# Kernel tuning notes

Hardware: AMD Instinct MI355X
Metric: run time of the kernel (lower is better)

The kernel has to match this reference:

```python
import jax, jax.numpy as jnp
import numpy as np

BN_EPS = 1e-5


def setup_inputs() -> dict:
    key = jax.random.key(0)
    k1, k2, k3 = jax.random.split(key, 3)
    B, T, V, Cin, Cout = 32, 256, 86, 64, 128
    x = jax.random.normal(k1, (B, T, V, Cin), dtype=jnp.float32)
    # random sparse symmetric 0/1 adjacency (no self loops; forward adds I)
    a = (jax.random.uniform(k2, (V, V)) < 0.08).astype(jnp.float32)
    adj = jnp.clip(a + a.T, 0.0, 1.0) * (1.0 - jnp.eye(V, dtype=jnp.float32))
    # kaiming_uniform_(a=sqrt(5)) on [Cin, Cout]: bound = sqrt(6/((1+5)*Cin)) = 1/sqrt(Cin)
    bound = 1.0 / np.sqrt(Cin)
    w = jax.random.uniform(k3, (Cin, Cout), minval=-bound, maxval=bound, dtype=jnp.float32)
    gamma = jnp.ones((Cout,), dtype=jnp.float32)
    beta = jnp.zeros((Cout,), dtype=jnp.float32)
    return {"x": x, "adj": adj, "w": w, "gamma": gamma, "beta": beta}


def reference(x, adj, w, gamma, beta):
    # x: [B, T, V, Cin]
    V = adj.shape[0]
    a = adj + jnp.eye(V, dtype=adj.dtype)
    deg_inv_sqrt = a.sum(axis=1) ** -0.5                      # [V]
    norm_adj = deg_inv_sqrt[:, None] * a * deg_inv_sqrt[None, :]
    # graph aggregation + feature transform (permute-free, fused einsums)
    y = jnp.einsum('uv,btvc->btuc', norm_adj, x)              # [B,T,V,Cin]
    y = jnp.einsum('btvc,cd->btvd', y, w)                     # [B,T,V,Cout]
    # BatchNorm2d (training mode): per-channel stats over (B,T,V)
    mean = y.mean(axis=(0, 1, 2))
    var = y.var(axis=(0, 1, 2))                               # biased, as in BN
    y = (y - mean) * jax.lax.rsqrt(var + BN_EPS) * gamma + beta
    return jax.nn.relu(y)                                     # [B,T,V,Cout]
```

## Files before the change

kernel.cpp:

```cpp
#include <hip/hip_runtime.h>

#define V 86
#define VP 96
#define CIN 64
#define COUT 128
#define BT 8192
#define NSTAT (32*256*86)

#define OFF_FLAG  0
#define OFF_NADJ  512
#define OFF_WT    19456
#define OFF_GSUM  35840
#define OFF_GSQ   36352
#define OFF_SCALE 36864
#define OFF_SHIFT 37376

typedef short short8 __attribute__((ext_vector_type(8)));
typedef float float4v __attribute__((ext_vector_type(4)));

static __device__ __forceinline__ float bf2f(ushort u) {
    union { uint i; float f; } c; c.i = ((uint)u) << 16; return c.f;
}
static __device__ __forceinline__ ushort f2bf(float f) {
    union { float f; uint i; } c; c.f = f;
    uint u = c.i;
    uint r = u + 0x7FFFu + ((u >> 16) & 1u);
    return (ushort)(r >> 16);
}
static __device__ __forceinline__ uint packbf(float a, float b) {
    return (uint)f2bf(a) | ((uint)f2bf(b) << 16);
}
template<bool BF>
static __device__ __forceinline__ float ldg(const void* p, int i) {
    if (BF) return bf2f(((const ushort*)p)[i]);
    else    return ((const float*)p)[i];
}

__global__ void k0_detect(const uint* __restrict__ adj_raw, char* __restrict__ ws) {
    __shared__ int s_found;
    if (threadIdx.x == 0) s_found = 0;
    __syncthreads();
    int found = 0;
    for (int i = threadIdx.x; i < 3698; i += blockDim.x) {
        uint wd = adj_raw[i];
        if (wd == 0x00003F80u || wd == 0x3F803F80u) found = 1;
    }
    if (found) atomicOr(&s_found, 1);
    __syncthreads();
    if (threadIdx.x == 0) *(int*)(ws + OFF_FLAG) = s_found;
}

template<bool BF>
__global__ void k1_prep(const void* __restrict__ adj, const void* __restrict__ w,
                        char* __restrict__ ws) {
    const int flag = *(const volatile int*)(ws + OFF_FLAG);
    if ((flag != 0) != BF) return;
    __shared__ float dinv[V];
    const int t = threadIdx.x;
    ushort* nadj = (ushort*)(ws + OFF_NADJ);
    ushort* wT   = (ushort*)(ws + OFF_WT);
    float*  gsum = (float*)(ws + OFF_GSUM);
    float*  gsq  = (float*)(ws + OFF_GSQ);

    if (t < V) {
        float s = 0.f;
        for (int v2 = 0; v2 < V; ++v2)
            s += ldg<BF>(adj, t * V + v2) + (v2 == t ? 1.f : 0.f);
        dinv[t] = rsqrtf(s);
    }
    __syncthreads();
    for (int i = t; i < VP * VP; i += blockDim.x) {
        int u = i / VP, v2 = i % VP;
        float val = 0.f;
        if (u < V && v2 < V) {
            float a = ldg<BF>(adj, u * V + v2) + (v2 == u ? 1.f : 0.f);
            val = dinv[u] * a * dinv[v2];
        }
        nadj[i] = f2bf(val);
    }
    for (int i = t; i < CIN * COUT; i += blockDim.x) {
        int cc = i >> 7, d = i & 127;
        wT[d * CIN + cc] = BF ? ((const ushort*)w)[i] : f2bf(((const float*)w)[i]);
    }
    if (t < COUT) { gsum[t] = 0.f; gsq[t] = 0.f; }
}

#define NJ_STR 104
#define XS_STR 72
#define YT_STR 104

template<bool BF, bool STATS>
__global__ __launch_bounds__(512, 4) void k2_pass(const void* __restrict__ x,
                                                  char* __restrict__ ws,
                                                  void* __restrict__ outv) {
    const int flag = *(const volatile int*)(ws + OFF_FLAG);
    if ((flag != 0) != BF) return;

    __shared__ __align__(16) short s_nadj[VP * NJ_STR];
    __shared__ __align__(16) short s_x[VP * XS_STR];
    __shared__ __align__(16) short s_yT[COUT * YT_STR];

    const int tid  = threadIdx.x;
    const int lane = tid & 63, wv = tid >> 6;
    const int col  = lane & 15, quad = lane >> 4;
    const int d_own = wv * 16 + col;

    {
        const ushort* g = (const ushort*)(ws + OFF_NADJ);
        for (int i = tid; i < VP * 12; i += 512) {
            int r = i / 12, j = i % 12;
            *(uint4*)&s_nadj[r * NJ_STR + j * 8] = *(const uint4*)&g[r * VP + j * 8];
        }
    }
    short8 bw[2];
    {
        const ushort* wt = (const ushort*)(ws + OFF_WT);
        bw[0] = *(const short8*)&wt[d_own * CIN + quad * 8];
        bw[1] = *(const short8*)&wt[d_own * CIN + 32 + quad * 8];
    }
    if (tid < 160) {
        int r = V + (tid >> 4), j = tid & 15;
        *(uint2*)&s_x[r * XS_STR + j * 4] = (uint2){0u, 0u};
    }
    float sc = 0.f, sh = 0.f;
    if (!STATS) {
        sc = ((const float*)(ws + OFF_SCALE))[d_own];
        sh = ((const float*)(ws + OFF_SHIFT))[d_own];
    }
    float s1 = 0.f, s2 = 0.f;

    for (int ib = 0; ib < 8; ++ib) {
        const int bt = blockIdx.x * 8 + ib;
        __syncthreads();

        if (BF) {
            const ushort* xg = (const ushort*)x + (size_t)bt * (V * CIN);
            for (int i = tid; i < V * 8; i += 512) {
                int r = i >> 3, j = i & 7;
                *(uint4*)&s_x[r * XS_STR + j * 8] = *(const uint4*)&xg[r * CIN + j * 8];
            }
        } else {
            const float* xg = (const float*)x + (size_t)bt * (V * CIN);
            for (int i = tid; i < V * 16; i += 512) {
                int r = i >> 4, j = i & 15;
                float4 f = *(const float4*)&xg[r * CIN + j * 4];
                uint2 o; o.x = packbf(f.x, f.y); o.y = packbf(f.z, f.w);
                *(uint2*)&s_x[r * XS_STR + j * 4] = o;
            }
        }
        __syncthreads();

        float4v accy[6];
        #pragma unroll
        for (int m = 0; m < 6; ++m) accy[m] = (float4v){0.f, 0.f, 0.f, 0.f};
        #pragma unroll
        for (int ks = 0; ks < 2; ++ks) {
            #pragma unroll
            for (int m = 0; m < 6; ++m) {
                short8 ax = *(const short8*)&s_x[(m * 16 + col) * XS_STR + ks * 32 + quad * 8];
                accy[m] = __builtin_amdgcn_mfma_f32_16x16x32_bf16(ax, bw[ks], accy[m], 0, 0, 0);
            }
        }
        #pragma unroll
        for (int m = 0; m < 6; ++m)
            #pragma unroll
            for (int r = 0; r < 4; ++r)
                s_yT[d_own * YT_STR + m * 16 + quad * 4 + r] = (short)f2bf(accy[m][r]);
        __syncthreads();

        float4v accz[6];
        #pragma unroll
        for (int m = 0; m < 6; ++m) accz[m] = (float4v){0.f, 0.f, 0.f, 0.f};
        #pragma unroll
        for (int ks = 0; ks < 3; ++ks) {
            short8 by = *(const short8*)&s_yT[d_own * YT_STR + ks * 32 + quad * 8];
            #pragma unroll
            for (int m = 0; m < 6; ++m) {
                short8 an = *(const short8*)&s_nadj[(m * 16 + col) * NJ_STR + ks * 32 + quad * 8];
                accz[m] = __builtin_amdgcn_mfma_f32_16x16x32_bf16(an, by, accz[m], 0, 0, 0);
            }
        }

        if (STATS) {
            #pragma unroll
            for (int m = 0; m < 6; ++m)
                #pragma unroll
                for (int r = 0; r < 4; ++r) {
                    int u = m * 16 + quad * 4 + r;
                    if (u < V) { float v2 = accz[m][r]; s1 += v2; s2 += v2 * v2; }
                }
        } else {
            const size_t base = (size_t)bt * (V * COUT) + d_own;
            #pragma unroll
            for (int m = 0; m < 6; ++m)
                #pragma unroll
                for (int r = 0; r < 4; ++r) {
                    int u = m * 16 + quad * 4 + r;
                    if (u < V) {
                        float val = fmaxf(accz[m][r] * sc + sh, 0.f);
                        if (BF) ((ushort*)outv)[base + (size_t)u * COUT] = f2bf(val);
                        else    ((float*)outv)[base + (size_t)u * COUT]  = val;
                    }
                }
        }
    }

    if (STATS) {
        s1 += __shfl_xor(s1, 16); s1 += __shfl_xor(s1, 32);
        s2 += __shfl_xor(s2, 16); s2 += __shfl_xor(s2, 32);
        if (quad == 0) {
            atomicAdd((float*)(ws + OFF_GSUM) + d_own, s1);
            atomicAdd((float*)(ws + OFF_GSQ)  + d_own, s2);
        }
    }
}

template<bool BF>
__global__ void k3_finalize(const void* __restrict__ gamma, const void* __restrict__ beta,
                            char* __restrict__ ws) {
    const int flag = *(const volatile int*)(ws + OFF_FLAG);
    if ((flag != 0) != BF) return;
    int d = threadIdx.x;
    if (d < COUT) {
        const float* gsum = (const float*)(ws + OFF_GSUM);
        const float* gsq  = (const float*)(ws + OFF_GSQ);
        float* scale = (float*)(ws + OFF_SCALE);
        float* shift = (float*)(ws + OFF_SHIFT);
        const float inv_n = 1.f / (float)NSTAT;
        float mean = gsum[d] * inv_n;
        float var  = gsq[d] * inv_n - mean * mean;
        float s    = ldg<BF>(gamma, d) * rsqrtf(var + 1e-5f);
        scale[d] = s;
        shift[d] = ldg<BF>(beta, d) - mean * s;
    }
}

extern "C" void kernel_launch(void* const* d_in, const int* in_sizes, int n_in,
                              void* d_out, int out_size, void* d_ws, size_t ws_size,
                              hipStream_t stream) {
    const void* x     = d_in[0];
    const void* adj   = d_in[1];
    const void* w     = d_in[2];
    const void* gamma = d_in[3];
    const void* beta  = d_in[4];
    char* ws = (char*)d_ws;

    hipLaunchKernelGGL(k0_detect, dim3(1), dim3(256), 0, stream, (const uint*)adj, ws);
    hipLaunchKernelGGL((k1_prep<true>),  dim3(1), dim3(256), 0, stream, adj, w, ws);
    hipLaunchKernelGGL((k1_prep<false>), dim3(1), dim3(256), 0, stream, adj, w, ws);
    hipLaunchKernelGGL((k2_pass<true,  true>),  dim3(1024), dim3(512), 0, stream, x, ws, d_out);
    hipLaunchKernelGGL((k2_pass<false, true>),  dim3(1024), dim3(512), 0, stream, x, ws, d_out);
    hipLaunchKernelGGL((k3_finalize<true>),  dim3(1), dim3(128), 0, stream, gamma, beta, ws);
    hipLaunchKernelGGL((k3_finalize<false>), dim3(1), dim3(128), 0, stream, gamma, beta, ws);
    hipLaunchKernelGGL((k2_pass<true,  false>), dim3(1024), dim3(512), 0, stream, x, ws, d_out);
    hipLaunchKernelGGL((k2_pass<false, false>), dim3(1024), dim3(512), 0, stream, x, ws, d_out);
}
```

Baseline: 613.7 us.

## Store pre-BN output in stats pass and apply BN in elementwise kernel

The stats pass now writes the raw aggregated-and-transformed values to the output buffer while accumulating channel statistics. A new vectorized elementwise kernel then applies scale, shift and ReLU in place. This replaces the second full recomputation pass, removing its re-read of x and its duplicate MFMA work. In exchange, the output is written and then read back and rewritten, which adds memory traffic.

```diff
diff --git a/kernel.cpp b/kernel.cpp
--- a/kernel.cpp
+++ b/kernel.cpp
@@ -4,7 +4,6 @@
 #define VP 96
 #define CIN 64
 #define COUT 128
-#define BT 8192
 #define NSTAT (32*256*86)
 
 #define OFF_FLAG  0
@@ -182,12 +181,18 @@
         }
 
         if (STATS) {
+            const size_t base = (size_t)bt * (V * COUT) + d_own;
             #pragma unroll
             for (int m = 0; m < 6; ++m)
                 #pragma unroll
                 for (int r = 0; r < 4; ++r) {
                     int u = m * 16 + quad * 4 + r;
-                    if (u < V) { float v2 = accz[m][r]; s1 += v2; s2 += v2 * v2; }
+                    if (u < V) {
+                        float v2 = accz[m][r];
+                        s1 += v2; s2 += v2 * v2;
+                        if (BF) ((ushort*)outv)[base + (size_t)u * COUT] = f2bf(v2);
+                        else    ((float*)outv)[base + (size_t)u * COUT]  = v2;
+                    }
                 }
         } else {
             const size_t base = (size_t)bt * (V * COUT) + d_own;
@@ -235,6 +240,55 @@
     }
 }
 
+template<bool BF>
+__global__ __launch_bounds__(256) void k4_bn(char* __restrict__ ws, void* __restrict__ outv) {
+    const int flag = *(const volatile int*)(ws + OFF_FLAG);
+    if ((flag != 0) != BF) return;
+    const float* scale = (const float*)(ws + OFF_SCALE);
+    const float* shift = (const float*)(ws + OFF_SHIFT);
+    const int d8 = threadIdx.x & 15;
+    float sc[8], sh[8];
+    #pragma unroll
+    for (int j = 0; j < 8; ++j) { sc[j] = scale[d8 * 8 + j]; sh[j] = shift[d8 * 8 + j]; }
+    const int nrows = 8192 * V;
+    const int rstride = (gridDim.x * blockDim.x) >> 4;
+    int row = (blockIdx.x * blockDim.x + threadIdx.x) >> 4;
+    for (; row < nrows; row += rstride) {
+        if (BF) {
+            uint4* p = (uint4*)((ushort*)outv + (size_t)row * COUT + d8 * 8);
+            uint4 v = *p;
+            float f0 = bf2f((ushort)v.x), f1 = bf2f((ushort)(v.x >> 16));
+            float f2 = bf2f((ushort)v.y), f3 = bf2f((ushort)(v.y >> 16));
+            float f4 = bf2f((ushort)v.z), f5 = bf2f((ushort)(v.z >> 16));
+            float f6 = bf2f((ushort)v.w), f7 = bf2f((ushort)(v.w >> 16));
+            f0 = fmaxf(fmaf(f0, sc[0], sh[0]), 0.f);
+            f1 = fmaxf(fmaf(f1, sc[1], sh[1]), 0.f);
+            f2 = fmaxf(fmaf(f2, sc[2], sh[2]), 0.f);
+            f3 = fmaxf(fmaf(f3, sc[3], sh[3]), 0.f);
+            f4 = fmaxf(fmaf(f4, sc[4], sh[4]), 0.f);
+            f5 = fmaxf(fmaf(f5, sc[5], sh[5]), 0.f);
+            f6 = fmaxf(fmaf(f6, sc[6], sh[6]), 0.f);
+            f7 = fmaxf(fmaf(f7, sc[7], sh[7]), 0.f);
+            uint4 o;
+            o.x = packbf(f0, f1); o.y = packbf(f2, f3);
+            o.z = packbf(f4, f5); o.w = packbf(f6, f7);
+            *p = o;
+        } else {
+            float4* p = (float4*)((float*)outv + (size_t)row * COUT + d8 * 8);
+            float4 a = p[0], b = p[1];
+            a.x = fmaxf(fmaf(a.x, sc[0], sh[0]), 0.f);
+            a.y = fmaxf(fmaf(a.y, sc[1], sh[1]), 0.f);
+            a.z = fmaxf(fmaf(a.z, sc[2], sh[2]), 0.f);
+            a.w = fmaxf(fmaf(a.w, sc[3], sh[3]), 0.f);
+            b.x = fmaxf(fmaf(b.x, sc[4], sh[4]), 0.f);
+            b.y = fmaxf(fmaf(b.y, sc[5], sh[5]), 0.f);
+            b.z = fmaxf(fmaf(b.z, sc[6], sh[6]), 0.f);
+            b.w = fmaxf(fmaf(b.w, sc[7], sh[7]), 0.f);
+            p[0] = a; p[1] = b;
+        }
+    }
+}
+
 extern "C" void kernel_launch(void* const* d_in, const int* in_sizes, int n_in,
                               void* d_out, int out_size, void* d_ws, size_t ws_size,
                               hipStream_t stream) {
@@ -252,6 +306,6 @@
     hipLaunchKernelGGL((k2_pass<false, true>),  dim3(1024), dim3(512), 0, stream, x, ws, d_out);
     hipLaunchKernelGGL((k3_finalize<true>),  dim3(1), dim3(128), 0, stream, gamma, beta, ws);
     hipLaunchKernelGGL((k3_finalize<false>), dim3(1), dim3(128), 0, stream, gamma, beta, ws);
-    hipLaunchKernelGGL((k2_pass<true,  false>), dim3(1024), dim3(512), 0, stream, x, ws, d_out);
-    hipLaunchKernelGGL((k2_pass<false, false>), dim3(1024), dim3(512), 0, stream, x, ws, d_out);
-}
+    hipLaunchKernelGGL((k4_bn<true>),  dim3(2048), dim3(256), 0, stream, ws, d_out);
+    hipLaunchKernelGGL((k4_bn<false>), dim3(2048), dim3(256), 0, stream, ws, d_out);
+}
```

New measurement: 691.6 us. 1.13x slower.

## Stage two time slices per barrier, drop intra-wave sync, skip unused dtype launches

Applied to the files above, without the earlier changes.

The main kernel now loads two (b,t) slices of x into a doubled shared buffer per iteration. This halves the outer loop count and its block-wide barriers. The barrier between writing and reading the transposed intermediate is removed, which relies on each wave touching only its own rows. The padding-row check in the stats accumulation is dropped because padded rows are zero. On the host, input byte sizes decide whether the bf16 or f32 kernel variants need launching, so launches that would return immediately are skipped. This saves launch overhead but raises shared memory use per block.

```diff
diff --git a/kernel.cpp b/kernel.cpp
--- a/kernel.cpp
+++ b/kernel.cpp
@@ -97,7 +97,7 @@
     if ((flag != 0) != BF) return;
 
     __shared__ __align__(16) short s_nadj[VP * NJ_STR];
-    __shared__ __align__(16) short s_x[VP * XS_STR];
+    __shared__ __align__(16) short s_x[2 * VP * XS_STR];
     __shared__ __align__(16) short s_yT[COUT * YT_STR];
 
     const int tid  = threadIdx.x;
@@ -121,6 +121,7 @@
     if (tid < 160) {
         int r = V + (tid >> 4), j = tid & 15;
         *(uint2*)&s_x[r * XS_STR + j * 4] = (uint2){0u, 0u};
+        *(uint2*)&s_x[VP * XS_STR + r * XS_STR + j * 4] = (uint2){0u, 0u};
     }
     float sc = 0.f, sh = 0.f;
     if (!STATS) {
@@ -129,79 +130,88 @@
     }
     float s1 = 0.f, s2 = 0.f;
 
-    for (int ib = 0; ib < 8; ++ib) {
-        const int bt = blockIdx.x * 8 + ib;
+    for (int ip = 0; ip < 4; ++ip) {
+        const int btp = blockIdx.x * 8 + ip * 2;
         __syncthreads();
 
-        if (BF) {
-            const ushort* xg = (const ushort*)x + (size_t)bt * (V * CIN);
-            for (int i = tid; i < V * 8; i += 512) {
-                int r = i >> 3, j = i & 7;
-                *(uint4*)&s_x[r * XS_STR + j * 8] = *(const uint4*)&xg[r * CIN + j * 8];
-            }
-        } else {
-            const float* xg = (const float*)x + (size_t)bt * (V * CIN);
-            for (int i = tid; i < V * 16; i += 512) {
-                int r = i >> 4, j = i & 15;
-                float4 f = *(const float4*)&xg[r * CIN + j * 4];
-                uint2 o; o.x = packbf(f.x, f.y); o.y = packbf(f.z, f.w);
-                *(uint2*)&s_x[r * XS_STR + j * 4] = o;
+        #pragma unroll
+        for (int h = 0; h < 2; ++h) {
+            short* sx = s_x + h * (VP * XS_STR);
+            if (BF) {
+                const ushort* xg = (const ushort*)x + (size_t)(btp + h) * (V * CIN);
+                for (int i = tid; i < V * 8; i += 512) {
+                    int r = i >> 3, j = i & 7;
+                    *(uint4*)&sx[r * XS_STR + j * 8] = *(const uint4*)&xg[r * CIN + j * 8];
+                }
+            } else {
+                const float* xg = (const float*)x + (size_t)(btp + h) * (V * CIN);
+                for (int i = tid; i < V * 16; i += 512) {
+                    int r = i >> 4, j = i & 15;
+                    float4 f = *(const float4*)&xg[r * CIN + j * 4];
+                    uint2 o; o.x = packbf(f.x, f.y); o.y = packbf(f.z, f.w);
+                    *(uint2*)&sx[r * XS_STR + j * 4] = o;
+                }
             }
         }
         __syncthreads();
 
-        float4v accy[6];
         #pragma unroll
-        for (int m = 0; m < 6; ++m) accy[m] = (float4v){0.f, 0.f, 0.f, 0.f};
-        #pragma unroll
-        for (int ks = 0; ks < 2; ++ks) {
-            #pragma unroll
-            for (int m = 0; m < 6; ++m) {
-                short8 ax = *(const short8*)&s_x[(m * 16 + col) * XS_STR + ks * 32 + quad * 8];
-                accy[m] = __builtin_amdgcn_mfma_f32_16x16x32_bf16(ax, bw[ks], accy[m], 0, 0, 0);
-            }
-        }
-        #pragma unroll
-        for (int m = 0; m < 6; ++m)
-            #pragma unroll
-            for (int r = 0; r < 4; ++r)
-                s_yT[d_own * YT_STR + m * 16 + quad * 4 + r] = (short)f2bf(accy[m][r]);
-        __syncthreads();
-
-        float4v accz[6];
-        #pragma unroll
-        for (int m = 0; m < 6; ++m) accz[m] = (float4v){0.f, 0.f, 0.f, 0.f};
-        #pragma unroll
-        for (int ks = 0; ks < 3; ++ks) {
-            short8 by = *(const short8*)&s_yT[d_own * YT_STR + ks * 32 + quad * 8];
-            #pragma unroll
-            for (int m = 0; m < 6; ++m) {
-                short8 an = *(const short8*)&s_nadj[(m * 16 + col) * NJ_STR + ks * 32 + quad * 8];
-                accz[m] = __builtin_amdgcn_mfma_f32_16x16x32_bf16(an, by, accz[m], 0, 0, 0);
-            }
-        }
-
-        if (STATS) {
+        for (int h = 0; h < 2; ++h) {
+            const short* sx = s_x + h * (VP * XS_STR);
+            const int bt = btp + h;
+
+            float4v accy[6];
+            #pragma unroll
+            for (int m = 0; m < 6; ++m) accy[m] = (float4v){0.f, 0.f, 0.f, 0.f};
+            #pragma unroll
+            for (int ks = 0; ks < 2; ++ks) {
+                #pragma unroll
+                for (int m = 0; m < 6; ++m) {
+                    short8 ax = *(const short8*)&sx[(m * 16 + col) * XS_STR + ks * 32 + quad * 8];
+                    accy[m] = __builtin_amdgcn_mfma_f32_16x16x32_bf16(ax, bw[ks], accy[m], 0, 0, 0);
+                }
+            }
             #pragma unroll
             for (int m = 0; m < 6; ++m)
                 #pragma unroll
-                for (int r = 0; r < 4; ++r) {
-                    int u = m * 16 + quad * 4 + r;
-                    if (u < V) { float v2 = accz[m][r]; s1 += v2; s2 += v2 * v2; }
-                }
-        } else {
-            const size_t base = (size_t)bt * (V * COUT) + d_own;
-            #pragma unroll
-            for (int m = 0; m < 6; ++m)
-                #pragma unroll
-                for (int r = 0; r < 4; ++r) {
-                    int u = m * 16 + quad * 4 + r;
-                    if (u < V) {
-                        float val = fmaxf(accz[m][r] * sc + sh, 0.f);
-                        if (BF) ((ushort*)outv)[base + (size_t)u * COUT] = f2bf(val);
-                        else    ((float*)outv)[base + (size_t)u * COUT]  = val;
+                for (int r = 0; r < 4; ++r)
+                    s_yT[d_own * YT_STR + m * 16 + quad * 4 + r] = (short)f2bf(accy[m][r]);
+
+            float4v accz[6];
+            #pragma unroll
+            for (int m = 0; m < 6; ++m) accz[m] = (float4v){0.f, 0.f, 0.f, 0.f};
+            #pragma unroll
+            for (int ks = 0; ks < 3; ++ks) {
+                short8 by = *(const short8*)&s_yT[d_own * YT_STR + ks * 32 + quad * 8];
+                #pragma unroll
+                for (int m = 0; m < 6; ++m) {
+                    short8 an = *(const short8*)&s_nadj[(m * 16 + col) * NJ_STR + ks * 32 + quad * 8];
+                    accz[m] = __builtin_amdgcn_mfma_f32_16x16x32_bf16(an, by, accz[m], 0, 0, 0);
+                }
+            }
+
+            if (STATS) {
+                #pragma unroll
+                for (int m = 0; m < 6; ++m)
+                    #pragma unroll
+                    for (int r = 0; r < 4; ++r) {
+                        float v2 = accz[m][r];
+                        s1 += v2; s2 += v2 * v2;
                     }
-                }
+            } else {
+                const size_t base = (size_t)bt * (V * COUT) + d_own;
+                #pragma unroll
+                for (int m = 0; m < 6; ++m)
+                    #pragma unroll
+                    for (int r = 0; r < 4; ++r) {
+                        int u = m * 16 + quad * 4 + r;
+                        if (u < V) {
+                            float val = fmaxf(accz[m][r] * sc + sh, 0.f);
+                            if (BF) ((ushort*)outv)[base + (size_t)u * COUT] = f2bf(val);
+                            else    ((float*)outv)[base + (size_t)u * COUT]  = val;
+                        }
+                    }
+            }
         }
     }
 
@@ -245,13 +255,18 @@
     const void* beta  = d_in[4];
     char* ws = (char*)d_ws;
 
+    const long long xb = (long long)in_sizes[0];
+    const long long ab = (long long)in_sizes[1];
+    const bool only_bf  = (ab == 86LL * 86 * 2) || (xb == 8192LL * 86 * 64 * 2);
+    const bool only_f32 = !only_bf && ((ab == 86LL * 86 * 4) || (xb == 8192LL * 86 * 64 * 4));
+
     hipLaunchKernelGGL(k0_detect, dim3(1), dim3(256), 0, stream, (const uint*)adj, ws);
-    hipLaunchKernelGGL((k1_prep<true>),  dim3(1), dim3(256), 0, stream, adj, w, ws);
-    hipLaunchKernelGGL((k1_prep<false>), dim3(1), dim3(256), 0, stream, adj, w, ws);
-    hipLaunchKernelGGL((k2_pass<true,  true>),  dim3(1024), dim3(512), 0, stream, x, ws, d_out);
-    hipLaunchKernelGGL((k2_pass<false, true>),  dim3(1024), dim3(512), 0, stream, x, ws, d_out);
-    hipLaunchKernelGGL((k3_finalize<true>),  dim3(1), dim3(128), 0, stream, gamma, beta, ws);
-    hipLaunchKernelGGL((k3_finalize<false>), dim3(1), dim3(128), 0, stream, gamma, beta, ws);
-    hipLaunchKernelGGL((k2_pass<true,  false>), dim3(1024), dim3(512), 0, stream, x, ws, d_out);
-    hipLaunchKernelGGL((k2_pass<false, false>), dim3(1024), dim3(512), 0, stream, x, ws, d_out);
-}
+    if (!only_f32) hipLaunchKernelGGL((k1_prep<true>),  dim3(1), dim3(256), 0, stream, adj, w, ws);
+    if (!only_bf)  hipLaunchKernelGGL((k1_prep<false>), dim3(1), dim3(256), 0, stream, adj, w, ws);
+    if (!only_f32) hipLaunchKernelGGL((k2_pass<true,  true>),  dim3(1024), dim3(512), 0, stream, x, ws, d_out);
+    if (!only_bf)  hipLaunchKernelGGL((k2_pass<false, true>),  dim3(1024), dim3(512), 0, stream, x, ws, d_out);
+    if (!only_f32) hipLaunchKernelGGL((k3_finalize<true>),  dim3(1), dim3(128), 0, stream, gamma, beta, ws);
+    if (!only_bf)  hipLaunchKernelGGL((k3_finalize<false>), dim3(1), dim3(128), 0, stream, gamma, beta, ws);
+    if (!only_f32) hipLaunchKernelGGL((k2_pass<true,  false>), dim3(1024), dim3(512), 0, stream, x, ws, d_out);
+    if (!only_bf)  hipLaunchKernelGGL((k2_pass<false, false>), dim3(1024), dim3(512), 0, stream, x, ws, d_out);
+}
```

After: 617.1 us. About the same (+0.6%).
